# Performance work log

Measured on AMD Instinct MI355X. Metric: run time of the kernel, lower is better.

## Reference

```python
import jax, jax.numpy as jnp
import numpy as np

B, S, N_CATE, N_CONT = 32, 1024, 4, 4
HIDDEN, ATTN, VOCAB, EMB = 1024, 512, 1000, 128


def sinusoidal_pe(seq_len, d_model, base=10000.0):
    pos = jnp.arange(seq_len, dtype=jnp.float32)[:, None]            # [S,1]
    i = jnp.arange(d_model // 2, dtype=jnp.float32)[None, :]         # [1,D/2]
    ang = pos / jnp.power(base, 2.0 * i / d_model)                   # [S,D/2]
    pe = jnp.zeros((seq_len, d_model), dtype=jnp.float32)
    pe = pe.at[:, 0::2].set(jnp.sin(ang))
    pe = pe.at[:, 1::2].set(jnp.cos(ang))
    return pe


def setup_inputs() -> dict:
    key = jax.random.key(0)
    ks = jax.random.split(key, 20)
    s = 0.02
    inp = {
        "cate_x": jax.random.randint(ks[0], (B, S, N_CATE), 0, VOCAB, dtype=jnp.int64)
                  if jax.config.read("jax_enable_x64") else
                  jax.random.randint(ks[0], (B, S, N_CATE), 0, VOCAB, dtype=jnp.int32),
        "cont_x": jax.random.normal(ks[1], (B, S, N_CONT), dtype=jnp.float32),
        "mask": jnp.ones((B, S), dtype=bool),
        "targets": jax.random.uniform(ks[2], (B, S), dtype=jnp.float32),
        # EntireEmbedding params: 4 cate tables + cont linear + comb projection
        "E0": jax.random.normal(ks[3], (VOCAB, EMB), dtype=jnp.float32) * s,
        "E1": jax.random.normal(ks[4], (VOCAB, EMB), dtype=jnp.float32) * s,
        "E2": jax.random.normal(ks[5], (VOCAB, EMB), dtype=jnp.float32) * s,
        "E3": jax.random.normal(ks[6], (VOCAB, EMB), dtype=jnp.float32) * s,
        "Wc": jax.random.normal(ks[7], (N_CONT, N_CATE * EMB), dtype=jnp.float32) * s,
        "Wproj": jax.random.normal(ks[8], (2 * N_CATE * EMB, HIDDEN), dtype=jnp.float32) * s,
        # two-head attention linears (bias=False)
        "WQ1": jax.random.normal(ks[9], (HIDDEN, ATTN), dtype=jnp.float32) * s,
        "WK1": jax.random.normal(ks[10], (HIDDEN, ATTN), dtype=jnp.float32) * s,
        "WV1": jax.random.normal(ks[11], (HIDDEN, ATTN), dtype=jnp.float32) * s,
        "WQ2": jax.random.normal(ks[12], (HIDDEN, ATTN), dtype=jnp.float32) * s,
        "WK2": jax.random.normal(ks[13], (HIDDEN, ATTN), dtype=jnp.float32) * s,
        "WV2": jax.random.normal(ks[14], (HIDDEN, ATTN), dtype=jnp.float32) * s,
        "W0": jax.random.normal(ks[15], (2 * ATTN, HIDDEN), dtype=jnp.float32) * s,
        "Wf": jax.random.normal(ks[16], (HIDDEN, 1), dtype=jnp.float32) * s,
    }
    return inp


def _attend(x, WQ, WK, WV):
    Q = x @ WQ  # [B,S,A]
    K = x @ WK
    V = x @ WV
    scores = jnp.einsum("bqd,bkd->bqk", Q, K) / jnp.sqrt(jnp.float32(ATTN))
    # faithful to nn.Softmax(dim=1): normalize over the QUERY axis
    attn = jax.nn.softmax(scores, axis=1)
    return jnp.einsum("bqk,bkv->bqv", attn, V)


def reference(cate_x, cont_x, mask, targets, E0, E1, E2, E3, Wc, Wproj,
              WQ1, WK1, WV1, WQ2, WK2, WV2, W0, Wf):
    # EntireEmbedding: per-feature cate embeddings + cont projection -> comb proj
    cate_emb = jnp.concatenate(
        [E0[cate_x[..., 0]], E1[cate_x[..., 1]], E2[cate_x[..., 2]], E3[cate_x[..., 3]]],
        axis=-1)                                   # [B,S,512]
    cont_emb = cont_x @ Wc                          # [B,S,512]
    x = jnp.concatenate([cate_emb, cont_emb], axis=-1) @ Wproj  # [B,S,H]
    x = x + sinusoidal_pe(x.shape[1], HIDDEN)[None, :, :]
    z1 = _attend(x, WQ1, WK1, WV1)                  # [B,S,A]
    z2 = _attend(x, WQ2, WK2, WV2)                  # [B,S,A]
    z = jnp.concatenate([z1, z2], axis=-1) @ W0     # [B,S,H]
    out = jax.nn.sigmoid(z @ Wf)                    # FinalConnecting: Linear(H,1)+sigmoid
    return out.squeeze(-1)                          # [B,S]
```

## Files before the change

kernel.cpp:

```cpp
#include <hip/hip_runtime.h>
#include <hip/hip_bf16.h>
#include <math.h>

#define BB    32
#define SS    1024
#define HID   1024
#define AT    512
#define NVOC  1000
#define NT    (BB*SS)

typedef unsigned short u16;
typedef __attribute__((ext_vector_type(8))) short s16x8;
typedef __attribute__((ext_vector_type(4))) float f32x4;

__device__ __forceinline__ float bf2f(u16 u) {
    union { unsigned int i; float f; } x; x.i = ((unsigned int)u) << 16; return x.f;
}
__device__ __forceinline__ u16 f2bf(float f) {
    union { float f; unsigned int i; } u; u.f = f;
    unsigned int r = u.i + 0x7fffu + ((u.i >> 16) & 1u);
    return (u16)(r >> 16);
}
__device__ __forceinline__ float4 ld4(const float* p) { return *(const float4*)p; }
__device__ __forceinline__ float4 ld4bf(const u16* p) {
    ushort4 v = *(const ushort4*)p;
    return make_float4(bf2f(v.x), bf2f(v.y), bf2f(v.z), bf2f(v.w));
}
__device__ __forceinline__ void unpack8(uint4 v, float* x) {
    x[0] = bf2f((u16)(v.x & 0xffff)); x[1] = bf2f((u16)(v.x >> 16));
    x[2] = bf2f((u16)(v.y & 0xffff)); x[3] = bf2f((u16)(v.y >> 16));
    x[4] = bf2f((u16)(v.z & 0xffff)); x[5] = bf2f((u16)(v.z >> 16));
    x[6] = bf2f((u16)(v.w & 0xffff)); x[7] = bf2f((u16)(v.w >> 16));
}

__device__ __forceinline__ void gld16(const u16* g, u16* l) {
    __builtin_amdgcn_global_load_lds(
        (const __attribute__((address_space(1))) unsigned int*)g,
        (__attribute__((address_space(3))) unsigned int*)l,
        16, 0, 0);
}

struct Ptrs4f { const float* p[4]; };

__device__ __forceinline__ float blockReduceSum(float x) {
    #pragma unroll
    for (int off = 32; off > 0; off >>= 1) x += __shfl_down(x, off, 64);
    __shared__ float tmp[4];
    int lane = threadIdx.x & 63, wid = threadIdx.x >> 6;
    if (lane == 0) tmp[wid] = x;
    __syncthreads();
    if (threadIdx.x == 0) x = tmp[0] + tmp[1] + tmp[2] + tmp[3];
    return x;
}
__device__ __forceinline__ float waveReduceSum(float x) {
    #pragma unroll
    for (int off = 32; off > 0; off >>= 1) x += __shfl_down(x, off, 64);
    return x;
}

__global__ void k_s1(Ptrs4f E, const float* __restrict__ Wproj, Ptrs4f W,
                     const float* __restrict__ W0, const float* __restrict__ Wf,
                     u16* __restrict__ PE16, u16* __restrict__ E16o, u16* __restrict__ Wp16,
                     u16* __restrict__ Wt, float* __restrict__ W0f,
                     float* __restrict__ Wcp, float* __restrict__ CQ) {
    int blk = blockIdx.x, tid = threadIdx.x;
    if (blk < 2048) {
        int idx = blk*256 + tid;
        int s = idx >> 9, i = idx & 511;
        const float l2_10000 = 13.287712379549449f;
        float denom = exp2f((2.f * (float)i / 1024.f) * l2_10000);
        float ang = (float)s / denom;
        unsigned int pack = ((unsigned int)f2bf(__cosf(ang)) << 16) | f2bf(__sinf(ang));
        *(unsigned int*)(PE16 + (size_t)s*1024 + 2*i) = pack;
    } else if (blk < 4048) {
        int id2 = blk - 2048;
        int f = id2 / 500;
        int i = (id2 % 500)*256 + tid;
        E16o[(size_t)f*128000 + i] = f2bf(E.p[f][i]);
    } else if (blk < 6096) {
        int i = (blk - 4048)*256 + tid;
        Wp16[i] = f2bf(Wproj[i]);
    } else if (blk < 8144) {
        int tb = blk - 6096;
        int mat = tb >> 9, t2 = tb & 511;
        int cx = t2 & 15, ry = t2 >> 4;
        int r0 = ry*32, c0 = cx*32;
        const float* in = W.p[mat];
        u16* out = Wt + (size_t)mat*1024*512;
        __shared__ float tt[32][33];
        int tx = tid & 31, ty8 = tid >> 5;
        #pragma unroll
        for (int it = 0; it < 4; ++it)
            tt[ty8 + it*8][tx] = in[(size_t)(r0 + ty8 + it*8)*512 + c0 + tx];
        __syncthreads();
        #pragma unroll
        for (int it = 0; it < 4; ++it)
            out[(size_t)(c0 + ty8 + it*8)*1024 + r0 + tx] = f2bf(tt[tx][ty8 + it*8]);
    } else if (blk < 9168) {
        int row = blk - 8144;
        const float* rp = W0 + (size_t)row*1024;
        float a = 0.f;
        for (int j = tid; j < 1024; j += 256) a += rp[j] * Wf[j];
        a = blockReduceSum(a);
        if (tid == 0) W0f[row] = a;
    } else {
        int idx = (blk - 9168)*256 + tid;
        if (idx < 4096) Wcp[idx] = 0.f;
        else CQ[idx - 4096] = 0.f;
    }
}

__global__ void k_s2(const float* __restrict__ Wc, const float* __restrict__ Wproj,
                     Ptrs4f W, const float* __restrict__ WV1, const float* __restrict__ WV2,
                     const float* __restrict__ W0f, float* __restrict__ Wcp, float* __restrict__ v) {
    int blk = blockIdx.x, tid = threadIdx.x;
    if (blk < 64) {
        int c = blk >> 4, ic = (blk >> 2) & 3, jc = blk & 3;
        int i = ic*256 + tid;
        float a = 0.f;
        for (int j = jc*128; j < jc*128 + 128; ++j)
            a += Wc[c*512 + j] * Wproj[(size_t)(512 + j)*1024 + i];
        atomicAdd(&Wcp[c*1024 + i], a);
    } else {
        int b2 = blk - 64;
        int h = b2 >> 10, i = b2 & 1023;
        const float* WV = h ? WV2 : WV1;
        const float* wf = W0f + h*512;
        float a = 0.f;
        for (int aa = tid; aa < 512; aa += 256) a += WV[(size_t)i*512 + aa] * wf[aa];
        a = blockReduceSum(a);
        if (tid == 0) v[h*1024 + i] = a;
    }
}

__device__ __forceinline__ void cstore(float* p, float v) { *p = v; }
__device__ __forceinline__ void cstore(u16* p, float v)   { *p = f2bf(v); }

template<typename CT, bool CTRANS>
__device__ __forceinline__ void mfma_gemm(const u16* __restrict__ A, const u16* __restrict__ B,
                                          CT* __restrict__ C, int M, int N, int K, float alpha,
                                          int m0, int n0) {
    __shared__ u16 As[128*64];
    __shared__ u16 Bs[128*64];
    const int tid = threadIdx.x;
    const int wave = tid >> 6, lane = tid & 63;
    const int quad = lane >> 4, l16 = lane & 15;
    const int wm = (wave >> 1)*64, wn = (wave & 1)*64;
    const int srow = lane >> 3;
    const int scol = ((lane & 7) ^ srow) * 8;
    f32x4 acc[4][4] = {};

    for (int k0 = 0; k0 < K; k0 += 64) {
        #pragma unroll
        for (int p = 0; p < 4; ++p) {
            int rb = wave*32 + p*8;
            gld16(A + (size_t)(m0 + rb + srow)*K + k0 + scol, As + rb*64);
            gld16(B + (size_t)(n0 + rb + srow)*K + k0 + scol, Bs + rb*64);
        }
        __syncthreads();
        #pragma unroll
        for (int kk = 0; kk < 2; ++kk) {
            s16x8 af[4], bf[4];
            #pragma unroll
            for (int i = 0; i < 4; ++i) {
                int row = wm + i*16 + l16;
                af[i] = *(const s16x8*)(As + row*64 + (((kk*4 + quad) ^ (row & 7)) * 8));
            }
            #pragma unroll
            for (int j = 0; j < 4; ++j) {
                int row = wn + j*16 + l16;
                bf[j] = *(const s16x8*)(Bs + row*64 + (((kk*4 + quad) ^ (row & 7)) * 8));
            }
            #pragma unroll
            for (int i = 0; i < 4; ++i)
                #pragma unroll
                for (int j = 0; j < 4; ++j)
                    acc[i][j] = __builtin_amdgcn_mfma_f32_16x16x32_bf16(af[i], bf[j], acc[i][j], 0, 0, 0);
        }
        __syncthreads();
    }
    #pragma unroll
    for (int i = 0; i < 4; ++i) {
        #pragma unroll
        for (int r = 0; r < 4; ++r) {
            int gm = m0 + wm + i*16 + quad*4 + r;
            if (gm < M) {
                #pragma unroll
                for (int j = 0; j < 4; ++j) {
                    int gn = n0 + wn + j*16 + l16;
                    if (CTRANS) cstore(C + (size_t)gn*M + gm, acc[i][j][r] * alpha);
                    else        cstore(C + (size_t)gm*N + gn, acc[i][j][r] * alpha);
                }
            }
        }
    }
}

__global__ __launch_bounds__(256) void k_s3(const u16* __restrict__ Wp16, const u16* __restrict__ Wt,
                                            u16* __restrict__ PWT,
                                            Ptrs4f W, const float* __restrict__ Wcp, float* __restrict__ CQ,
                                            const float* __restrict__ Wproj, const float* __restrict__ v,
                                            float* __restrict__ pv) {
    int blk = blockIdx.x, tid = threadIdx.x;
    if (blk < 64) {
        int x = blk & 3, z = blk >> 2;
        int f = z >> 2, w = z & 3;
        mfma_gemm<u16,true>(Wp16 + (size_t)f*128*1024, Wt + (size_t)w*512*1024,
                            PWT + (size_t)z*512*128, 128, 512, 1024, 1.f, 0, x*128);
    } else if (blk < 320) {
        int r = blk - 64;
        int ns = r & 1, wc = (r >> 1) & 15, jc = r >> 5;
        int w = wc & 3, c = wc >> 2; int n = ns*256 + tid;
        const float* Ww = W.p[w];
        float a = 0.f;
        for (int j = jc*128; j < jc*128 + 128; ++j) a += Wcp[c*1024 + j] * Ww[(size_t)j*512 + n];
        atomicAdd(&CQ[(size_t)(w*4 + c)*512 + n], a);
    } else {
        int b2 = blk - 320;
        int i = b2 & 127, fh = b2 >> 7; int f = fh >> 1, h = fh & 1;
        const float* row = Wproj + (size_t)(f*128 + i)*1024;
        const float* vh = v + h*1024;
        float a = 0.f;
        for (int j = tid; j < 1024; j += 256) a += row[j] * vh[j];
        a = blockReduceSum(a);
        if (tid == 0) pv[(size_t)fh*128 + i] = a;
    }
}

__global__ __launch_bounds__(256) void k_s4(const u16* __restrict__ E16, const u16* __restrict__ PWT,
                                            const u16* __restrict__ PE16, const u16* __restrict__ Wt,
                                            u16* __restrict__ TQK16, u16* __restrict__ PEQ16,
                                            const float* __restrict__ Wcp, const float* __restrict__ v,
                                            const float* __restrict__ pv,
                                            float* __restrict__ Ut, float* __restrict__ pu, float* __restrict__ cu) {
    int blk = blockIdx.x;
    if (blk < 640) {
        int z = blk >> 5, r = blk & 31, y = r >> 2, x = r & 3;
        if (z < 16) {
            int f = z >> 2;
            mfma_gemm<u16,false>(E16 + (size_t)f*128000, PWT + (size_t)z*512*128,
                       TQK16 + (size_t)z*1000*512, 1000, 512, 128, 1.f, y*128, x*128);
        } else {
            int w = z - 16;
            mfma_gemm<u16,false>(PE16, Wt + (size_t)w*512*1024, PEQ16 + (size_t)w*1024*512,
                       1024, 512, 1024, 1.f, y*128, x*128);
        }
        return;
    }
    int id = blk - 640;
    if (id < 2000) {
        int wave = threadIdx.x >> 6, lane = threadIdx.x & 63;
        int d = id*4 + wave;
        int f = d / 2000, h = (d / 1000) & 1, r = d % 1000;
        unsigned int e2 = *(const unsigned int*)(E16 + ((size_t)f*1000 + r)*128 + lane*2);
        const float* pvp = pv + (size_t)(f*2 + h)*128 + lane*2;
        float a = bf2f((u16)(e2 & 0xffff)) * pvp[0] + bf2f((u16)(e2 >> 16)) * pvp[1];
        a = waveReduceSum(a);
        if (lane == 0) Ut[(size_t)(f*2 + h)*1000 + r] = a;
    } else if (id < 4048) {
        int tq = id - 2000; int h = tq >> 10, s = tq & 1023;
        float4 a = ld4bf(PE16 + (size_t)s*1024 + threadIdx.x*4);
        float4 b = ld4(v + h*1024 + threadIdx.x*4);
        float p = a.x*b.x + a.y*b.y + a.z*b.z + a.w*b.w;
        p = blockReduceSum(p);
        if (threadIdx.x == 0) pu[h*1024 + s] = p;
    } else {
        int tq = id - 4048; int h = tq >> 2, c = tq & 3;
        float4 a = ld4(Wcp + c*1024 + threadIdx.x*4);
        float4 b = ld4(v + h*1024 + threadIdx.x*4);
        float p = a.x*b.x + a.y*b.y + a.z*b.z + a.w*b.w;
        p = blockReduceSum(p);
        if (threadIdx.x == 0) cu[h*4 + c] = p;
    }
}

__global__ __launch_bounds__(512, 2) void k_g_S256(
        const u16* __restrict__ Q, const u16* __restrict__ K,
        u16* __restrict__ Sb, float alpha,
        float* __restrict__ Pm, float* __restrict__ Pd, int b0) {
    __shared__ u16 As[2][16384];
    __shared__ u16 Bs[2][16384];
    const int tid = threadIdx.x;
    const int wave = tid >> 6, lane = tid & 63;
    const int quad = lane >> 4, l16 = lane & 15;
    const int wm = wave >> 2, wn = wave & 3;

    const int nwg = (int)gridDim.x;
    int fblk = (int)blockIdx.x;
    int qq = nwg >> 3, rr = nwg & 7;
    int xcd = fblk & 7, idx = fblk >> 3;
    int swz = (xcd < rr ? xcd*(qq + 1) : rr*(qq + 1) + (xcd - rr)*qq) + idx;
    int b = swz >> 4, tile = swz & 15;
    int m0 = (tile >> 2) << 8, n0 = (tile & 3) << 8;

    const u16* __restrict__ Ab = Q + (size_t)b*SS*AT;
    const u16* __restrict__ Bb = K + (size_t)b*SS*AT;
    u16* __restrict__ C = Sb + (size_t)b*SS*SS;

    const int srow = lane >> 3;
    const int scol = ((lane & 7) ^ srow) * 8;

    f32x4 acc[8][4] = {};

    auto stageA = [&](int kt, int q) {
        gld16(Ab + (size_t)(m0 + q*64 + wave*8 + srow)*AT + kt*64 + scol,
              &As[kt & 1][q*4096 + wave*512]);
    };
    auto stageB = [&](int kt, int q) {
        gld16(Bb + (size_t)(n0 + q*64 + wave*8 + srow)*AT + kt*64 + scol,
              &Bs[kt & 1][q*4096 + wave*512]);
    };

    s16x8 af[4][2];
    s16x8 bf[4][2];

    auto readA = [&](int c, int ih) {
        #pragma unroll
        for (int i2 = 0; i2 < 4; ++i2) {
            int row = wm*128 + (ih*4 + i2)*16 + l16;
            #pragma unroll
            for (int kk = 0; kk < 2; ++kk)
                af[i2][kk] = *(const s16x8*)(&As[c][row*64 + (((kk*4 + quad) ^ (row & 7)) * 8)]);
        }
    };
    auto readB2 = [&](int c, int jh) {
        #pragma unroll
        for (int j2 = 0; j2 < 2; ++j2) {
            int j = jh*2 + j2;
            int row = wn*64 + j*16 + l16;
            #pragma unroll
            for (int kk = 0; kk < 2; ++kk)
                bf[j][kk] = *(const s16x8*)(&Bs[c][row*64 + (((kk*4 + quad) ^ (row & 7)) * 8)]);
        }
    };
    auto mma16 = [&](int ih, int jh) {
        __builtin_amdgcn_s_setprio(1);
        #pragma unroll
        for (int i2 = 0; i2 < 4; ++i2)
            #pragma unroll
            for (int j2 = 0; j2 < 2; ++j2) {
                int i = ih*4 + i2, j = jh*2 + j2;
                acc[i][j] = __builtin_amdgcn_mfma_f32_16x16x32_bf16(af[i2][0], bf[j][0], acc[i][j], 0, 0, 0);
                acc[i][j] = __builtin_amdgcn_mfma_f32_16x16x32_bf16(af[i2][1], bf[j][1], acc[i][j], 0, 0, 0);
            }
        __builtin_amdgcn_s_setprio(0);
    };
    auto midsync = [&]() {
        __builtin_amdgcn_s_barrier();
        asm volatile("s_waitcnt lgkmcnt(0)" ::: "memory");
        __builtin_amdgcn_sched_barrier(0);
    };

    #pragma unroll
    for (int q = 0; q < 4; ++q) stageA(0, q);
    #pragma unroll
    for (int q = 0; q < 4; ++q) stageB(0, q);
    stageA(1, 0); stageA(1, 2);
    stageB(1, 0); stageB(1, 1); stageB(1, 2); stageB(1, 3);
    asm volatile("s_waitcnt vmcnt(6)" ::: "memory");
    __builtin_amdgcn_s_barrier();

    #pragma unroll
    for (int t = 0; t < 8; ++t) {
        const int c = t & 1;
        readA(c, 0);
        readB2(c, 0);
        if (t <= 6) { stageA(t + 1, 1); stageA(t + 1, 3); }
        midsync();
        mma16(0, 0);
        __builtin_amdgcn_s_barrier();
        readB2(c, 1);
        if (t <= 5) { stageA(t + 2, 0); stageA(t + 2, 2); }
        midsync();
        mma16(0, 1);
        __builtin_amdgcn_s_barrier();
        readA(c, 1);
        if (t <= 5) { stageB(t + 2, 0); stageB(t + 2, 1); }
        midsync();
        mma16(1, 0);
        __builtin_amdgcn_s_barrier();
        if (t <= 5) { stageB(t + 2, 2); stageB(t + 2, 3); }
        midsync();
        mma16(1, 1);
        if (t <= 5)      asm volatile("s_waitcnt vmcnt(6)" ::: "memory");
        else if (t == 6) asm volatile("s_waitcnt vmcnt(0)" ::: "memory");
        __builtin_amdgcn_sched_barrier(0);
        __builtin_amdgcn_s_barrier();
    }

    #pragma unroll
    for (int i = 0; i < 8; ++i) {
        #pragma unroll
        for (int r = 0; r < 4; ++r) {
            int gm = m0 + wm*128 + i*16 + quad*4 + r;
            u16 q0 = f2bf(acc[i][0][r] * alpha);
            u16 q1 = f2bf(acc[i][1][r] * alpha);
            u16 q2 = f2bf(acc[i][2][r] * alpha);
            u16 q3 = f2bf(acc[i][3][r] * alpha);
            acc[i][0][r] = bf2f(q0); acc[i][1][r] = bf2f(q1);
            acc[i][2][r] = bf2f(q2); acc[i][3][r] = bf2f(q3);
            unsigned int lo = (unsigned int)q0 | ((unsigned int)q1 << 16);
            unsigned int hi = (unsigned int)q2 | ((unsigned int)q3 << 16);
            *(uint2*)(C + (size_t)gm*SS + n0 + wn*64 + l16*4) = make_uint2(lo, hi);
        }
    }
    float* sM = (float*)&As[0][0];
    float* sS = (float*)&Bs[0][0];
    #pragma unroll
    for (int j = 0; j < 4; ++j) {
        float mx = -3.4e38f;
        #pragma unroll
        for (int i = 0; i < 8; ++i)
            #pragma unroll
            for (int r = 0; r < 4; ++r) mx = fmaxf(mx, acc[i][j][r]);
        mx = fmaxf(mx, __shfl_xor(mx, 16, 64));
        mx = fmaxf(mx, __shfl_xor(mx, 32, 64));
        float sm = 0.f;
        #pragma unroll
        for (int i = 0; i < 8; ++i)
            #pragma unroll
            for (int r = 0; r < 4; ++r) sm += exp2f(acc[i][j][r] - mx);
        sm += __shfl_xor(sm, 16, 64);
        sm += __shfl_xor(sm, 32, 64);
        if (quad == 0) { sM[wave*64 + j*16 + l16] = mx; sS[wave*64 + j*16 + l16] = sm; }
    }
    __syncthreads();
    if (tid < 256) {
        int c = tid, wq = c >> 6, cc = c & 63;
        float ma = sM[wq*64 + cc],       sa = sS[wq*64 + cc];
        float mb = sM[(4 + wq)*64 + cc], sb2 = sS[(4 + wq)*64 + cc];
        float mm = fmaxf(ma, mb);
        float ss = sa * exp2f(ma - mm) + sb2 * exp2f(mb - mm);
        size_t po = ((size_t)(b0 + b)*4 + (m0 >> 8))*1024;
        Pm[po + n0 + c] = mm;
        Pd[po + n0 + c] = ss;
    }
}

__global__ __launch_bounds__(256) void k_gather(
                         const int* __restrict__ cate, const float* __restrict__ cont,
                         const u16* __restrict__ TQK, const float* __restrict__ CQ,
                         const u16* __restrict__ PEQ, const float* __restrict__ Ut,
                         const float* __restrict__ cu, const float* __restrict__ pu,
                         u16* __restrict__ Qh, u16* __restrict__ Kh,
                         float* __restrict__ u, int h) {
    int tid = threadIdx.x;
    int g = blockIdx.x & 7;
    size_t t = (size_t)(blockIdx.x >> 3)*16 + (tid >> 4);
    int e = (tid >> 3) & 1;
    int cslot = tid & 7;
    int s = (int)(t & 1023);
    int4 cc = *(const int4*)(cate + t*4);
    float4 cv = ld4(cont + t*4);
    int w = 2*h + e;
    int n = g*64 + cslot*8;
    const u16* t0 = TQK + ((size_t)(0*4  + w)*1000 + cc.x)*512 + n;
    const u16* t1 = TQK + ((size_t)(1*4  + w)*1000 + cc.y)*512 + n;
    const u16* t2 = TQK + ((size_t)(2*4  + w)*1000 + cc.z)*512 + n;
    const u16* t3 = TQK + ((size_t)(3*4  + w)*1000 + cc.w)*512 + n;
    const u16* pq = PEQ + ((size_t)w*1024 + s)*512 + n;
    const float* cq = CQ + (size_t)w*2048 + n;
    float a0[8], a1[8], a2[8], a3[8], ap[8];
    unpack8(*(const uint4*)t0, a0); unpack8(*(const uint4*)t1, a1);
    unpack8(*(const uint4*)t2, a2); unpack8(*(const uint4*)t3, a3);
    unpack8(*(const uint4*)pq, ap);
    unsigned int pack[4];
    #pragma unroll
    for (int jp = 0; jp < 4; ++jp) {
        float x0, x1;
        #pragma unroll
        for (int half = 0; half < 2; ++half) {
            int j = jp*2 + half;
            float x = a0[j] + a1[j] + a2[j] + a3[j] + ap[j]
                    + cv.x*cq[j] + cv.y*cq[512+j] + cv.z*cq[1024+j] + cv.w*cq[1536+j];
            if (half == 0) x0 = x; else x1 = x;
        }
        pack[jp] = ((unsigned int)f2bf(x1) << 16) | f2bf(x0);
    }
    u16* op = (e ? Kh : Qh) + t*512 + n;
    *(uint4*)op = make_uint4(pack[0], pack[1], pack[2], pack[3]);
    if (g == 0 && (tid & 15) == 0) {
        float uu = pu[h*1024 + s]
                 + Ut[(0*2 + h)*1000 + cc.x] + Ut[(1*2 + h)*1000 + cc.y]
                 + Ut[(2*2 + h)*1000 + cc.z] + Ut[(3*2 + h)*1000 + cc.w]
                 + cv.x*cu[h*4+0] + cv.y*cu[h*4+1] + cv.z*cu[h*4+2] + cv.w*cu[h*4+3];
        u[(size_t)h*NT + t] = uu;
    }
}

__global__ void k_stats_combine(const float* __restrict__ Pm, const float* __restrict__ Pd,
                                const float* __restrict__ u, float* __restrict__ wexp, int b0) {
    int idx = b0*1024 + blockIdx.x*256 + threadIdx.x;
    int b = idx >> 10, k = idx & 1023;
    float mx = -3.4e38f;
    #pragma unroll
    for (int mt = 0; mt < 4; ++mt) mx = fmaxf(mx, Pm[((size_t)b*4 + mt)*1024 + k]);
    float dd = 0.f;
    #pragma unroll
    for (int mt = 0; mt < 4; ++mt) dd += Pd[((size_t)b*4 + mt)*1024 + k]
                                       * exp2f(Pm[((size_t)b*4 + mt)*1024 + k] - mx);
    int q = (k & ~63) | (((k & 15) << 2) | ((k & 63) >> 4));
    wexp[((size_t)b << 10) + q] = u[idx] / dd * exp2f(-mx);
}

__global__ void k_logit(const u16* __restrict__ Sb, const float* __restrict__ wexp,
                        float* __restrict__ logits, float* __restrict__ out,
                        int b0, int mode) {
    int wave = threadIdx.x >> 6, lane = threadIdx.x & 63;
    size_t bi = (size_t)(gridDim.x - 1 - blockIdx.x);
    size_t tl = bi*4 + wave;
    size_t tabs = (size_t)b0*1024 + tl;
    int b = (int)(tabs >> 10);
    const u16* row = Sb + tl*1024;
    const float* wb = wexp + ((size_t)b << 10);
    float acc = 0.f;
    #pragma unroll
    for (int half = 0; half < 2; ++half) {
        int k = lane*8 + half*512;
        float sv[8];
        unpack8(*(const uint4*)(row + k), sv);
        float4 w0 = ld4(wb + k), w1 = ld4(wb + k + 4);
        acc += exp2f(sv[0])*w0.x + exp2f(sv[1])*w0.y + exp2f(sv[2])*w0.z + exp2f(sv[3])*w0.w
             + exp2f(sv[4])*w1.x + exp2f(sv[5])*w1.y + exp2f(sv[6])*w1.z + exp2f(sv[7])*w1.w;
    }
    acc = waveReduceSum(acc);
    if (lane == 0) {
        if (mode == 0) logits[tabs] = acc;
        else {
            float x = logits[tabs] + acc;
            out[tabs] = 1.f / (1.f + expf(-x));
        }
    }
}

extern "C" void kernel_launch(void* const* d_in, const int* in_sizes, int n_in,
                              void* d_out, int out_size, void* d_ws, size_t ws_size,
                              hipStream_t stream) {
    const int*   cate = (const int*)d_in[0];
    const float* cont = (const float*)d_in[1];
    Ptrs4f E; E.p[0] = (const float*)d_in[4]; E.p[1] = (const float*)d_in[5];
              E.p[2] = (const float*)d_in[6]; E.p[3] = (const float*)d_in[7];
    const float* Wc    = (const float*)d_in[8];
    const float* Wproj = (const float*)d_in[9];
    Ptrs4f W; W.p[0] = (const float*)d_in[10];
              W.p[1] = (const float*)d_in[11];
              W.p[2] = (const float*)d_in[13];
              W.p[3] = (const float*)d_in[14];
    const float* WV1 = (const float*)d_in[12];
    const float* WV2 = (const float*)d_in[15];
    const float* W0  = (const float*)d_in[16];
    const float* Wf  = (const float*)d_in[17];

    char* base = (char*)d_ws;
    size_t off = 0;
    auto alloc = [&](size_t bytes) { void* p = base + off; off += (bytes + 255) & ~(size_t)255; return p; };
    u16*   PE16  = (u16*)  alloc(1048576ull*2);
    u16*   E16   = (u16*)  alloc(4ull*1000*128*2);
    u16*   Wt    = (u16*)  alloc(4ull*512*1024*2);
    u16*   Wp16  = (u16*)  alloc(512ull*1024*2);
    u16*   PWT   = (u16*)  alloc(16ull*512*128*2);
    u16*   TQK16 = (u16*)  alloc(16ull*1000*512*2);
    u16*   PEQ16 = (u16*)  alloc(4ull*1024*512*2);
    float* Wcp   = (float*)alloc(4*1024*4);
    float* W0f   = (float*)alloc(1024*4);
    float* vv    = (float*)alloc(2*1024*4);
    float* CQ    = (float*)alloc(16*512*4);
    float* pvb   = (float*)alloc(8*128*4);
    float* Ut    = (float*)alloc(8*1000*4);
    float* cu    = (float*)alloc(8*4);
    float* pu    = (float*)alloc(2*1024*4);
    float* ubuf  = (float*)alloc(2ull*NT*4);
    u16*   Qh    = (u16*)  alloc((size_t)NT*512*2);
    u16*   Kh    = (u16*)  alloc((size_t)NT*512*2);
    float* Pm    = (float*)alloc(32ull*8*1024*4);
    float* Pd    = (float*)alloc(32ull*8*1024*4);
    float* wbuf  = (float*)alloc(32*1024*4);
    float* logits= (float*)alloc((size_t)NT*4);
    size_t sChunkBytes = (size_t)SS*SS*2;
    size_t remain = (ws_size > off) ? (ws_size - off) : 0;
    int NB = (int)(remain / sChunkBytes);
    if (NB > 32) NB = 32;
    if (NB < 1) NB = 1;
    u16* Sbuf = (u16*)(base + off);

    const float alpha = 0.06375954951107036f;

    k_s1<<<9216, 256, 0, stream>>>(E, Wproj, W, W0, Wf, PE16, E16, Wp16, Wt, W0f, Wcp, CQ);
    k_s2<<<2112, 256, 0, stream>>>(Wc, Wproj, W, WV1, WV2, W0f, Wcp, vv);
    k_s3<<<1344, 256, 0, stream>>>(Wp16, Wt, PWT, W, Wcp, CQ, Wproj, vv, pvb);
    k_s4<<<4696, 256, 0, stream>>>(E16, PWT, PE16, Wt, TQK16, PEQ16, Wcp, vv, pvb, Ut, pu, cu);

    for (int h = 0; h < 2; ++h) {
        k_gather<<<16384, 256, 0, stream>>>(cate, cont, TQK16, CQ, PEQ16, Ut, cu, pu, Qh, Kh, ubuf, h);
        for (int b0 = 0; b0 < 32; b0 += NB) {
            int nb = (32 - b0 < NB) ? (32 - b0) : NB;
            k_g_S256<<<16*nb, 512, 0, stream>>>(Qh + (size_t)b0*SS*AT, Kh + (size_t)b0*SS*AT,
                                                Sbuf, alpha, Pm, Pd, b0);
            k_stats_combine<<<nb*4, 256, 0, stream>>>(Pm, Pd, ubuf + (size_t)h*NT, wbuf, b0);
            k_logit<<<nb*256, 256, 0, stream>>>(Sbuf, wbuf, logits, (float*)d_out, b0, h);
        }
    }
}
```

Baseline: 344.8 us.

## Fuse softmax stats combine into logit kernel and move PE GEMM to stage 3

```diff
diff --git a/kernel.cpp b/kernel.cpp
--- a/kernel.cpp
+++ b/kernel.cpp
@@ -198,6 +198,7 @@
 
 __global__ __launch_bounds__(256) void k_s3(const u16* __restrict__ Wp16, const u16* __restrict__ Wt,
                                             u16* __restrict__ PWT,
+                                            const u16* __restrict__ PE16, u16* __restrict__ PEQ16,
                                             Ptrs4f W, const float* __restrict__ Wcp, float* __restrict__ CQ,
                                             const float* __restrict__ Wproj, const float* __restrict__ v,
                                             float* __restrict__ pv) {
@@ -207,8 +208,13 @@
         int f = z >> 2, w = z & 3;
         mfma_gemm<u16,true>(Wp16 + (size_t)f*128*1024, Wt + (size_t)w*512*1024,
                             PWT + (size_t)z*512*128, 128, 512, 1024, 1.f, 0, x*128);
-    } else if (blk < 320) {
-        int r = blk - 64;
+    } else if (blk < 192) {
+        int idx = blk - 64;
+        int w = idx >> 5, r2 = idx & 31, y = r2 >> 2, x = r2 & 3;
+        mfma_gemm<u16,false>(PE16, Wt + (size_t)w*512*1024, PEQ16 + (size_t)w*1024*512,
+                             1024, 512, 1024, 1.f, y*128, x*128);
+    } else if (blk < 448) {
+        int r = blk - 192;
         int ns = r & 1, wc = (r >> 1) & 15, jc = r >> 5;
         int w = wc & 3, c = wc >> 2; int n = ns*256 + tid;
         const float* Ww = W.p[w];
@@ -216,7 +222,7 @@
         for (int j = jc*128; j < jc*128 + 128; ++j) a += Wcp[c*1024 + j] * Ww[(size_t)j*512 + n];
         atomicAdd(&CQ[(size_t)(w*4 + c)*512 + n], a);
     } else {
-        int b2 = blk - 320;
+        int b2 = blk - 448;
         int i = b2 & 127, fh = b2 >> 7; int f = fh >> 1, h = fh & 1;
         const float* row = Wproj + (size_t)(f*128 + i)*1024;
         const float* vh = v + h*1024;
@@ -228,26 +234,20 @@
 }
 
 __global__ __launch_bounds__(256) void k_s4(const u16* __restrict__ E16, const u16* __restrict__ PWT,
-                                            const u16* __restrict__ PE16, const u16* __restrict__ Wt,
-                                            u16* __restrict__ TQK16, u16* __restrict__ PEQ16,
+                                            const u16* __restrict__ PE16,
+                                            u16* __restrict__ TQK16,
                                             const float* __restrict__ Wcp, const float* __restrict__ v,
                                             const float* __restrict__ pv,
                                             float* __restrict__ Ut, float* __restrict__ pu, float* __restrict__ cu) {
     int blk = blockIdx.x;
-    if (blk < 640) {
+    if (blk < 512) {
         int z = blk >> 5, r = blk & 31, y = r >> 2, x = r & 3;
-        if (z < 16) {
-            int f = z >> 2;
-            mfma_gemm<u16,false>(E16 + (size_t)f*128000, PWT + (size_t)z*512*128,
-                       TQK16 + (size_t)z*1000*512, 1000, 512, 128, 1.f, y*128, x*128);
-        } else {
-            int w = z - 16;
-            mfma_gemm<u16,false>(PE16, Wt + (size_t)w*512*1024, PEQ16 + (size_t)w*1024*512,
-                       1024, 512, 1024, 1.f, y*128, x*128);
-        }
+        int f = z >> 2;
+        mfma_gemm<u16,false>(E16 + (size_t)f*128000, PWT + (size_t)z*512*128,
+                   TQK16 + (size_t)z*1000*512, 1000, 512, 128, 1.f, y*128, x*128);
         return;
     }
-    int id = blk - 640;
+    int id = blk - 512;
     if (id < 2000) {
         int wave = threadIdx.x >> 6, lane = threadIdx.x & 63;
         int d = id*4 + wave;
@@ -488,38 +488,40 @@
     }
 }
 
-__global__ void k_stats_combine(const float* __restrict__ Pm, const float* __restrict__ Pd,
-                                const float* __restrict__ u, float* __restrict__ wexp, int b0) {
-    int idx = b0*1024 + blockIdx.x*256 + threadIdx.x;
-    int b = idx >> 10, k = idx & 1023;
-    float mx = -3.4e38f;
-    #pragma unroll
-    for (int mt = 0; mt < 4; ++mt) mx = fmaxf(mx, Pm[((size_t)b*4 + mt)*1024 + k]);
-    float dd = 0.f;
-    #pragma unroll
-    for (int mt = 0; mt < 4; ++mt) dd += Pd[((size_t)b*4 + mt)*1024 + k]
-                                       * exp2f(Pm[((size_t)b*4 + mt)*1024 + k] - mx);
-    int q = (k & ~63) | (((k & 15) << 2) | ((k & 63) >> 4));
-    wexp[((size_t)b << 10) + q] = u[idx] / dd * exp2f(-mx);
-}
-
-__global__ void k_logit(const u16* __restrict__ Sb, const float* __restrict__ wexp,
+__global__ __launch_bounds__(1024) void k_logit(const u16* __restrict__ Sb,
+                        const float* __restrict__ Pm, const float* __restrict__ Pd,
+                        const float* __restrict__ u,
                         float* __restrict__ logits, float* __restrict__ out,
                         int b0, int mode) {
+    __shared__ float wsm[1024];
     int wave = threadIdx.x >> 6, lane = threadIdx.x & 63;
     size_t bi = (size_t)(gridDim.x - 1 - blockIdx.x);
-    size_t tl = bi*4 + wave;
-    size_t tabs = (size_t)b0*1024 + tl;
-    int b = (int)(tabs >> 10);
+    size_t tl0 = bi*16;
+    size_t tabs0 = (size_t)b0*1024 + tl0;
+    int ab = (int)(tabs0 >> 10);
+    {
+        int k = threadIdx.x;
+        float mx = -3.4e38f;
+        #pragma unroll
+        for (int mt = 0; mt < 4; ++mt) mx = fmaxf(mx, Pm[((size_t)ab*4 + mt)*1024 + k]);
+        float dd = 0.f;
+        #pragma unroll
+        for (int mt = 0; mt < 4; ++mt) dd += Pd[((size_t)ab*4 + mt)*1024 + k]
+                                           * exp2f(Pm[((size_t)ab*4 + mt)*1024 + k] - mx);
+        int q = (k & ~63) | (((k & 15) << 2) | ((k & 63) >> 4));
+        wsm[q] = u[(size_t)ab*1024 + k] / dd * exp2f(-mx);
+    }
+    __syncthreads();
+    size_t tl = tl0 + wave;
+    size_t tabs = tabs0 + wave;
     const u16* row = Sb + tl*1024;
-    const float* wb = wexp + ((size_t)b << 10);
     float acc = 0.f;
     #pragma unroll
     for (int half = 0; half < 2; ++half) {
         int k = lane*8 + half*512;
         float sv[8];
         unpack8(*(const uint4*)(row + k), sv);
-        float4 w0 = ld4(wb + k), w1 = ld4(wb + k + 4);
+        float4 w0 = ld4(wsm + k), w1 = ld4(wsm + k + 4);
         acc += exp2f(sv[0])*w0.x + exp2f(sv[1])*w0.y + exp2f(sv[2])*w0.z + exp2f(sv[3])*w0.w
              + exp2f(sv[4])*w1.x + exp2f(sv[5])*w1.y + exp2f(sv[6])*w1.z + exp2f(sv[7])*w1.w;
     }
@@ -574,7 +576,6 @@
     u16*   Kh    = (u16*)  alloc((size_t)NT*512*2);
     float* Pm    = (float*)alloc(32ull*8*1024*4);
     float* Pd    = (float*)alloc(32ull*8*1024*4);
-    float* wbuf  = (float*)alloc(32*1024*4);
     float* logits= (float*)alloc((size_t)NT*4);
     size_t sChunkBytes = (size_t)SS*SS*2;
     size_t remain = (ws_size > off) ? (ws_size - off) : 0;
@@ -587,8 +588,8 @@
 
     k_s1<<<9216, 256, 0, stream>>>(E, Wproj, W, W0, Wf, PE16, E16, Wp16, Wt, W0f, Wcp, CQ);
     k_s2<<<2112, 256, 0, stream>>>(Wc, Wproj, W, WV1, WV2, W0f, Wcp, vv);
-    k_s3<<<1344, 256, 0, stream>>>(Wp16, Wt, PWT, W, Wcp, CQ, Wproj, vv, pvb);
-    k_s4<<<4696, 256, 0, stream>>>(E16, PWT, PE16, Wt, TQK16, PEQ16, Wcp, vv, pvb, Ut, pu, cu);
+    k_s3<<<1472, 256, 0, stream>>>(Wp16, Wt, PWT, PE16, PEQ16, W, Wcp, CQ, Wproj, vv, pvb);
+    k_s4<<<4568, 256, 0, stream>>>(E16, PWT, PE16, TQK16, Wcp, vv, pvb, Ut, pu, cu);
 
     for (int h = 0; h < 2; ++h) {
         k_gather<<<16384, 256, 0, stream>>>(cate, cont, TQK16, CQ, PEQ16, Ut, cu, pu, Qh, Kh, ubuf, h);
@@ -596,8 +597,8 @@
             int nb = (32 - b0 < NB) ? (32 - b0) : NB;
             k_g_S256<<<16*nb, 512, 0, stream>>>(Qh + (size_t)b0*SS*AT, Kh + (size_t)b0*SS*AT,
                                                 Sbuf, alpha, Pm, Pd, b0);
-            k_stats_combine<<<nb*4, 256, 0, stream>>>(Pm, Pd, ubuf + (size_t)h*NT, wbuf, b0);
-            k_logit<<<nb*256, 256, 0, stream>>>(Sbuf, wbuf, logits, (float*)d_out, b0, h);
-        }
-    }
-}
+            k_logit<<<nb*64, 1024, 0, stream>>>(Sbuf, Pm, Pd, ubuf + (size_t)h*NT,
+                                                logits, (float*)d_out, b0, h);
+        }
+    }
+}
```

Result: faster. 336.7 us (-2.4%).
